# Kernel optimization log

Measured on AMD Instinct MI355X. Metric: run time of the kernel, lower is better.

Reference implementation:

```python
import jax, jax.numpy as jnp
import numpy as np

LEVELS = 2
_H0 = jnp.array([0.0322231, -0.01260397, -0.09921954, 0.2978578,
                 0.80373875, 0.49761867, -0.02963553, -0.07576571], dtype=jnp.float32)
_H1 = _H0[::-1] * jnp.array([-1.0, 1.0] * 4, dtype=jnp.float32)  # db4 QMF


def subband_conv2d(x, kernel_2d, stride):
    # depthwise grouped conv: same 2D kernel applied to every channel
    C = x.shape[-1]
    k = jnp.tile(kernel_2d[:, :, None, None], (1, 1, 1, C))  # HWIO with I=1, groups=C
    return jax.lax.conv_general_dilated(
        x, k, window_strides=(stride, stride), padding='SAME',
        dimension_numbers=('NHWC', 'HWIO', 'NHWC'), feature_group_count=C)


def _upsample2d(t):
    B, H, W, C = t.shape
    return jnp.zeros((B, 2 * H, 2 * W, C), t.dtype).at[:, ::2, ::2, :].set(t)


def _local_conv(t, w):
    # per-spatial-position linear map over channels: [B,H,W,I] x [I,O,W,H] -> [B,H,W,O]
    return jnp.einsum('bhwi,iowh->bhwo', t, w)


def setup_inputs() -> dict:
    key = jax.random.key(0)
    ks = jax.random.split(key, 9)
    B, H, W, C, O = 16, 128, 128, 64, 64
    inp = {
        'x': jax.random.normal(ks[0], (B, H, W, C), dtype=jnp.float32),
        'wLL': 0.02 * jax.random.normal(ks[1], (C, O, 32, 32), dtype=jnp.float32),
        'wLH_l0': 0.02 * jax.random.normal(ks[2], (C, O, 64, 64), dtype=jnp.float32),
        'wHL_l0': 0.02 * jax.random.normal(ks[3], (C, O, 64, 64), dtype=jnp.float32),
        'wHH_l0': 0.02 * jax.random.normal(ks[4], (C, O, 64, 64), dtype=jnp.float32),
        'wLH_l1': 0.02 * jax.random.normal(ks[5], (C, O, 32, 32), dtype=jnp.float32),
        'wHL_l1': 0.02 * jax.random.normal(ks[6], (C, O, 32, 32), dtype=jnp.float32),
        'wHH_l1': 0.02 * jax.random.normal(ks[7], (C, O, 32, 32), dtype=jnp.float32),
    }
    return inp


def reference(x, wLL, wLH_l0, wHL_l0, wHH_l0, wLH_l1, wHL_l1, wHH_l1):
    h0, h1 = _H0, _H1
    g0, g1 = h0[::-1], h1[::-1]
    # H=W=128 is divisible by 2**levels, so no symmetric padding is needed.
    res = x
    details = []
    for _ in range(LEVELS):
        cLL = subband_conv2d(res, jnp.outer(h0, h0), 2)
        cLH = subband_conv2d(res, jnp.outer(h0, h1), 2)
        cHL = subband_conv2d(res, jnp.outer(h1, h0), 2)
        cHH = subband_conv2d(res, jnp.outer(h1, h1), 2)
        details.append((cLH, cHL, cHH))
        res = cLL
    yA = _local_conv(res, wLL)  # [B,32,32,O]
    det_w = [(wLH_l0, wHL_l0, wHH_l0), (wLH_l1, wHL_l1, wHH_l1)]
    td = []
    for i in range(LEVELS):
        lh, hl, hh = details[i]
        wlh, whl, whh = det_w[i]
        td.append((_local_conv(lh, wlh), _local_conv(hl, whl), _local_conv(hh, whh)))
    r = yA
    for i in reversed(range(LEVELS)):
        yLH, yHL, yHH = td[i]
        r = (subband_conv2d(_upsample2d(r), jnp.outer(g0, g0), 1)
             + subband_conv2d(_upsample2d(yLH), jnp.outer(g0, g1), 1)
             + subband_conv2d(_upsample2d(yHL), jnp.outer(g1, g0), 1)
             + subband_conv2d(_upsample2d(yHH), jnp.outer(g1, g1), 1))
    return r
```

## Files before the change

### kernel.cpp

```cpp
#include <hip/hip_runtime.h>

__device__ __constant__ float H0[8] = { 0.0322231f, -0.01260397f, -0.09921954f,  0.2978578f,
                                        0.80373875f, 0.49761867f, -0.02963553f, -0.07576571f};
__device__ __constant__ float H1[8] = { 0.07576571f, -0.02963553f, -0.49761867f, 0.80373875f,
                                       -0.2978578f, -0.09921954f,  0.01260397f,  0.0322231f};
__device__ __constant__ float G0[8] = {-0.07576571f, -0.02963553f,  0.49761867f, 0.80373875f,
                                        0.2978578f,  -0.09921954f, -0.01260397f, 0.0322231f};
__device__ __constant__ float G1[8] = { 0.0322231f,   0.01260397f, -0.09921954f, -0.2978578f,
                                        0.80373875f, -0.49761867f, -0.02963553f, 0.07576571f};

template<int HIN>
__global__ __launch_bounds__(256) void fwd_dwt(const float* __restrict__ in,
                                               float* __restrict__ oLL, float* __restrict__ oLH,
                                               float* __restrict__ oHL, float* __restrict__ oHH)
{
    constexpr int OH = HIN / 2;
    constexpr int TQ = OH / 2;
    const int tid = threadIdx.x;
    const int c = tid & 63;
    const int s = blockIdx.x * 4 + (tid >> 6);
    const int j = s % TQ;
    const int i = (s / TQ) % TQ;
    const int b = s / (TQ * TQ);

    float acc[2][2][4];
#pragma unroll
    for (int a = 0; a < 2; ++a)
#pragma unroll
        for (int d = 0; d < 2; ++d)
#pragma unroll
            for (int k = 0; k < 4; ++k) acc[a][d][k] = 0.f;

    const int iw0 = 4 * j - 3;
#pragma unroll
    for (int r = 0; r < 10; ++r) {
        const int ih = 4 * i + r - 3;
        if ((unsigned)ih < (unsigned)HIN) {
            const float* row = in + ((b * HIN + ih) * HIN) * 64 + c;
            float xv[10];
#pragma unroll
            for (int v = 0; v < 10; ++v) {
                const int iw = iw0 + v;
                xv[v] = ((unsigned)iw < (unsigned)HIN) ? row[iw * 64] : 0.f;
            }
            float h00 = 0.f, h01 = 0.f, h10 = 0.f, h11 = 0.f;
#pragma unroll
            for (int v = 0; v < 8; ++v) {
                h00 += H0[v] * xv[v];
                h10 += H1[v] * xv[v];
                h01 += H0[v] * xv[v + 2];
                h11 += H1[v] * xv[v + 2];
            }
#pragma unroll
            for (int ii = 0; ii < 2; ++ii) {
                const int u = r - 2 * ii;
                if (0 <= u && u < 8) {
                    const float a0 = H0[u], a1 = H1[u];
                    acc[ii][0][0] += a0 * h00;
                    acc[ii][0][1] += a0 * h10;
                    acc[ii][0][2] += a1 * h00;
                    acc[ii][0][3] += a1 * h10;
                    acc[ii][1][0] += a0 * h01;
                    acc[ii][1][1] += a0 * h11;
                    acc[ii][1][2] += a1 * h01;
                    acc[ii][1][3] += a1 * h11;
                }
            }
        }
    }

#pragma unroll
    for (int ii = 0; ii < 2; ++ii)
#pragma unroll
        for (int jj = 0; jj < 2; ++jj) {
            const int oh = 2 * i + ii, ow = 2 * j + jj;
            const int oidx = ((b * OH + oh) * OH + ow) * 64 + c;
            oLL[oidx] = acc[ii][jj][0];
            oLH[oidx] = acc[ii][jj][1];
            oHL[oidx] = acc[ii][jj][2];
            oHH[oidx] = acc[ii][jj][3];
        }
}

template<int HD>
__global__ __launch_bounds__(256) void act_tr(const float* __restrict__ in,
                                              float* __restrict__ outp)
{
    __shared__ float Ld[64][HD + 1];
    const int w = blockIdx.x;
    const int b = blockIdx.y;
    const int t = threadIdx.x;

    {
        const int i = t & 63;
        const int hq = t >> 6;
#pragma unroll
        for (int s = 0; s < HD / 4; ++s) {
            const int h = hq * (HD / 4) + s;
            Ld[i][h] = in[((size_t)(b * HD + h) * HD + w) * 64 + i];
        }
    }
    __syncthreads();
    {
        const int h = t & (HD - 1);
        const int iq = t / HD;
        constexpr int NIQ = 256 / HD;
#pragma unroll
        for (int s = 0; s < 64 / NIQ; ++s) {
            const int i = s * NIQ + iq;
            outp[((size_t)(w * 64 + i) * 16 + b) * HD + h] = Ld[i][h];
        }
    }
}

template<int HD, int OT, int HG>
__global__ __launch_bounds__(256, 4) void local_conv_t(
    const float* __restrict__ a0, const float* __restrict__ a1,
    const float* __restrict__ a2, const float* __restrict__ a3,
    const float* __restrict__ w0, const float* __restrict__ w1,
    const float* __restrict__ w2, const float* __restrict__ w3,
    float* __restrict__ o0, float* __restrict__ o1,
    float* __restrict__ o2, float* __restrict__ o3)
{
    constexpr int WH   = HD * HD;
    constexpr int NO   = OT / 4;
    constexpr int WL   = OT / 8;
    constexpr int LOG2OT = (OT == 32) ? 5 : 4;
    constexpr int RSW  = OT + 4;
    constexpr int RSA  = 20;

    __shared__ __align__(16) float Wl[4][32][RSW];
    __shared__ __align__(16) float Al[4][32][RSA];

    const int z = blockIdx.z;
    const float* act = (z == 0) ? a0 : (z == 1) ? a1 : (z == 2) ? a2 : a3;
    const float* wgt = (z == 0) ? w0 : (z == 1) ? w1 : (z == 2) ? w2 : w3;
    float*       out = (z == 0) ? o0 : (z == 1) ? o1 : (z == 2) ? o2 : o3;

    const int bx    = blockIdx.x;
    const int hg    = bx % HG;
    const int og    = bx / HG;
    const int hbase = hg * 32;
    const int w     = blockIdx.y;
    const int t     = threadIdx.x;

    int whq[WL], wot[WL], wii[WL];
#pragma unroll
    for (int l = 0; l < WL; ++l) {
        const int idx = t + 256 * l;
        whq[l] = idx & 7;
        wot[l] = (idx >> 3) & (OT - 1);
        wii[l] = idx >> (3 + LOG2OT);
    }
    const int ahq = t & 7, ab = (t >> 3) & 15, aii0 = t >> 7;

    const int hc = t & 31;
    const int r  = t >> 5;
    const int oo = r & 3;
    const int bq = r >> 2;

    float4 acc4[8][NO / 4];
#pragma unroll
    for (int j = 0; j < 8; ++j)
#pragma unroll
        for (int q = 0; q < NO / 4; ++q) acc4[j][q] = make_float4(0.f, 0.f, 0.f, 0.f);

    float4 wv[WL], av[2];
#pragma unroll
    for (int l = 0; l < WL; ++l)
        wv[l] = *(const float4*)(wgt + (size_t)(wii[l] * 64 + og * OT + wot[l]) * WH
                                 + w * HD + hbase + whq[l] * 4);
#pragma unroll
    for (int l = 0; l < 2; ++l)
        av[l] = *(const float4*)(act + (size_t)((w * 64 + aii0 + 2 * l) * 16 + ab) * HD
                                 + hbase + ahq * 4);

    for (int chunk = 0; chunk < 16; ++chunk) {
        __syncthreads();
#pragma unroll
        for (int l = 0; l < WL; ++l) {
            Wl[wii[l]][whq[l] * 4 + 0][wot[l]] = wv[l].x;
            Wl[wii[l]][whq[l] * 4 + 1][wot[l]] = wv[l].y;
            Wl[wii[l]][whq[l] * 4 + 2][wot[l]] = wv[l].z;
            Wl[wii[l]][whq[l] * 4 + 3][wot[l]] = wv[l].w;
        }
#pragma unroll
        for (int l = 0; l < 2; ++l) {
            const int ii = aii0 + 2 * l;
            Al[ii][ahq * 4 + 0][ab] = av[l].x;
            Al[ii][ahq * 4 + 1][ab] = av[l].y;
            Al[ii][ahq * 4 + 2][ab] = av[l].z;
            Al[ii][ahq * 4 + 3][ab] = av[l].w;
        }
        __syncthreads();

        if (chunk < 15) {
            const int i0n = (chunk + 1) * 4;
#pragma unroll
            for (int l = 0; l < WL; ++l)
                wv[l] = *(const float4*)(wgt + (size_t)((i0n + wii[l]) * 64 + og * OT + wot[l]) * WH
                                         + w * HD + hbase + whq[l] * 4);
#pragma unroll
            for (int l = 0; l < 2; ++l)
                av[l] = *(const float4*)(act + (size_t)((w * 64 + i0n + aii0 + 2 * l) * 16 + ab) * HD
                                         + hbase + ahq * 4);
        }

#pragma unroll
        for (int ii = 0; ii < 4; ++ii) {
            float4 wf[NO / 4];
#pragma unroll
            for (int q = 0; q < NO / 4; ++q)
                wf[q] = *(const float4*)&Wl[ii][hc][oo * NO + q * 4];
            float4 af0 = *(const float4*)&Al[ii][hc][bq * 8];
            float4 af1 = *(const float4*)&Al[ii][hc][bq * 8 + 4];
            const float* afp0 = (const float*)&af0;
            const float* afp1 = (const float*)&af1;
#pragma unroll
            for (int j = 0; j < 4; ++j) {
                const float aa = afp0[j];
#pragma unroll
                for (int q = 0; q < NO / 4; ++q) {
                    acc4[j][q].x += aa * wf[q].x;
                    acc4[j][q].y += aa * wf[q].y;
                    acc4[j][q].z += aa * wf[q].z;
                    acc4[j][q].w += aa * wf[q].w;
                }
            }
#pragma unroll
            for (int j = 0; j < 4; ++j) {
                const float aa = afp1[j];
#pragma unroll
                for (int q = 0; q < NO / 4; ++q) {
                    acc4[j + 4][q].x += aa * wf[q].x;
                    acc4[j + 4][q].y += aa * wf[q].y;
                    acc4[j + 4][q].z += aa * wf[q].z;
                    acc4[j + 4][q].w += aa * wf[q].w;
                }
            }
        }
    }

#pragma unroll
    for (int j = 0; j < 8; ++j) {
        const int b = bq * 8 + j;
        float* op = out + ((size_t)(b * HD + hbase + hc) * HD + w) * 64 + og * OT + oo * NO;
#pragma unroll
        for (int q = 0; q < NO / 4; ++q)
            *(float4*)(op + q * 4) = acc4[j][q];
    }
}

template<int HOUT>
__global__ __launch_bounds__(256) void inv_dwt(const float* __restrict__ yLL,
                                               const float* __restrict__ yLH,
                                               const float* __restrict__ yHL,
                                               const float* __restrict__ yHH,
                                               float* __restrict__ out)
{
    constexpr int HS = HOUT / 2;
    const int tid = threadIdx.x;
    const int c = tid & 63;
    const int s = blockIdx.x * 4 + (tid >> 6);
    const int j = s % HS;
    const int i = (s / HS) % HS;
    const int b = s / (HS * HS);

    float Pe[4] = {0.f, 0.f, 0.f, 0.f}, Po[4] = {0.f, 0.f, 0.f, 0.f};
    float Qe[4] = {0.f, 0.f, 0.f, 0.f}, Qo[4] = {0.f, 0.f, 0.f, 0.f};

#pragma unroll
    for (int ku = 0; ku < 4; ++ku) {
        const int m = i - 1 + ku;
        if ((unsigned)m < (unsigned)HS) {
            const float a0e = G0[1 + 2 * ku], a0o = G0[2 * ku];
            const float a1e = G1[1 + 2 * ku], a1o = G1[2 * ku];
            const int rowoff = (b * HS + m) * HS;
#pragma unroll
            for (int kv = 0; kv < 4; ++kv) {
                const int n = j - 1 + kv;
                if ((unsigned)n < (unsigned)HS) {
                    const int idx = (rowoff + n) * 64 + c;
                    const float yll = yLL[idx], ylh = yLH[idx];
                    const float yhl = yHL[idx], yhh = yHH[idx];
                    Pe[kv] += a0e * yll + a1e * yhl;
                    Po[kv] += a0o * yll + a1o * yhl;
                    Qe[kv] += a0e * ylh + a1e * yhh;
                    Qo[kv] += a0o * ylh + a1o * yhh;
                }
            }
        }
    }

    float o00 = 0.f, o01 = 0.f, o10 = 0.f, o11 = 0.f;
#pragma unroll
    for (int kv = 0; kv < 4; ++kv) {
        const float b0e = G0[1 + 2 * kv], b0o = G0[2 * kv];
        const float b1e = G1[1 + 2 * kv], b1o = G1[2 * kv];
        o00 += b0e * Pe[kv] + b1e * Qe[kv];
        o01 += b0o * Pe[kv] + b1o * Qe[kv];
        o10 += b0e * Po[kv] + b1e * Qo[kv];
        o11 += b0o * Po[kv] + b1o * Qo[kv];
    }

    const int h0 = 2 * i, w0 = 2 * j;
    const int base = ((b * HOUT + h0) * HOUT + w0) * 64 + c;
    out[base] = o00;
    out[base + 64] = o01;
    out[base + HOUT * 64] = o10;
    out[base + HOUT * 64 + 64] = o11;
}

extern "C" void kernel_launch(void* const* d_in, const int* in_sizes, int n_in,
                              void* d_out, int out_size, void* d_ws, size_t ws_size,
                              hipStream_t stream)
{
    const float* x    = (const float*)d_in[0];
    const float* wLL  = (const float*)d_in[1];
    const float* wLH0 = (const float*)d_in[2];
    const float* wHL0 = (const float*)d_in[3];
    const float* wHH0 = (const float*)d_in[4];
    const float* wLH1 = (const float*)d_in[5];
    const float* wHL1 = (const float*)d_in[6];
    const float* wHH1 = (const float*)d_in[7];
    float* out = (float*)d_out;
    float* ws  = (float*)d_ws;

    const int S0 = 16 * 64 * 64 * 64;
    const int S1 = 16 * 32 * 32 * 64;

    float* c0 = out;
    float* A0 = out;
    float* A1 = out + 3 * S0;

    float* c1 = ws;
    float* t0 = ws + 4 * S1;
    float* t1 = ws + 4 * S1 + 3 * S0;
    float* yA = ws + 7 * S1 + 3 * S0;
    float* r1 = ws;

    fwd_dwt<128><<<16 * 32 * 32 / 4, 256, 0, stream>>>(x, c0, c0 + S0, c0 + 2 * S0, c0 + 3 * S0);

    fwd_dwt<64><<<16 * 16 * 16 / 4, 256, 0, stream>>>(c0,
        c1 + 0 * S1, c1 + 1 * S1, c1 + 2 * S1, c1 + 3 * S1);

    act_tr<64><<<dim3(64, 16), 256, 0, stream>>>(c0 + 1 * S0, A0 + 0 * S0);
    act_tr<64><<<dim3(64, 16), 256, 0, stream>>>(c0 + 2 * S0, A0 + 1 * S0);
    act_tr<64><<<dim3(64, 16), 256, 0, stream>>>(c0 + 3 * S0, A0 + 2 * S0);

    act_tr<32><<<dim3(32, 16), 256, 0, stream>>>(c1 + 0 * S1, A1 + 0 * S1);
    act_tr<32><<<dim3(32, 16), 256, 0, stream>>>(c1 + 1 * S1, A1 + 1 * S1);
    act_tr<32><<<dim3(32, 16), 256, 0, stream>>>(c1 + 2 * S1, A1 + 2 * S1);
    act_tr<32><<<dim3(32, 16), 256, 0, stream>>>(c1 + 3 * S1, A1 + 3 * S1);

    local_conv_t<64, 32, 2><<<dim3(4, 64, 3), 256, 0, stream>>>(
        A0 + 0 * S0, A0 + 1 * S0, A0 + 2 * S0, nullptr,
        wLH0, wHL0, wHH0, nullptr,
        t0 + 0 * S0, t0 + 1 * S0, t0 + 2 * S0, nullptr);

    local_conv_t<32, 16, 1><<<dim3(4, 32, 4), 256, 0, stream>>>(
        A1 + 1 * S1, A1 + 2 * S1, A1 + 3 * S1, A1 + 0 * S1,
        wLH1, wHL1, wHH1, wLL,
        t1 + 0 * S1, t1 + 1 * S1, t1 + 2 * S1, yA);

    inv_dwt<64><<<16 * 32 * 32 / 4, 256, 0, stream>>>(
        yA, t1 + 0 * S1, t1 + 1 * S1, t1 + 2 * S1, r1);

    inv_dwt<128><<<16 * 64 * 64 / 4, 256, 0, stream>>>(
        r1, t0 + 0 * S0, t0 + 1 * S0, t0 + 2 * S0, out);
}
```

Baseline: 333.0 us.

## Replace LDS-staged local conv with direct register loads and LDS-transposed stores

The per-position channel-mixing kernel no longer stages weight and activation tiles through shared memory with double-buffered prefetch. Each thread now loads its weights and activations straight from global memory with coalesced scalar loads along h and accumulates in registers. The result is transposed through a padded shared buffer so output stores stay coalesced. Level-0 output tiling drops from 32 to 16 channels per block, doubling the grid. This removes LDS traffic and per-chunk barriers, but loses register-level data reuse and the overlap of loads with compute.

```diff
diff --git a/kernel.cpp b/kernel.cpp
--- a/kernel.cpp
+++ b/kernel.cpp
@@ -114,7 +114,7 @@
 }
 
 template<int HD, int OT, int HG>
-__global__ __launch_bounds__(256, 4) void local_conv_t(
+__global__ __launch_bounds__(256) void local_conv_direct(
     const float* __restrict__ a0, const float* __restrict__ a1,
     const float* __restrict__ a2, const float* __restrict__ a3,
     const float* __restrict__ w0, const float* __restrict__ w1,
@@ -122,15 +122,15 @@
     float* __restrict__ o0, float* __restrict__ o1,
     float* __restrict__ o2, float* __restrict__ o3)
 {
-    constexpr int WH   = HD * HD;
-    constexpr int NO   = OT / 4;
-    constexpr int WL   = OT / 8;
-    constexpr int LOG2OT = (OT == 32) ? 5 : 4;
-    constexpr int RSW  = OT + 4;
-    constexpr int RSA  = 20;
-
-    __shared__ __align__(16) float Wl[4][32][RSW];
-    __shared__ __align__(16) float Al[4][32][RSA];
+    constexpr int WH  = HD * HD;
+    constexpr int NOO = OT / 8;
+    constexpr int NBQ = 8 / NOO;
+    constexpr int NB  = 16 / NBQ;
+    constexpr int NO4 = OT / 4;
+    constexpr int NEX = 256 / (NO4 * 32);
+    constexpr int NF  = NB / NEX;
+
+    __shared__ float E[NB][32][33];
 
     const int z = blockIdx.z;
     const float* act = (z == 0) ? a0 : (z == 1) ? a1 : (z == 2) ? a2 : a3;
@@ -144,110 +144,67 @@
     const int w     = blockIdx.y;
     const int t     = threadIdx.x;
 
-    int whq[WL], wot[WL], wii[WL];
-#pragma unroll
-    for (int l = 0; l < WL; ++l) {
-        const int idx = t + 256 * l;
-        whq[l] = idx & 7;
-        wot[l] = (idx >> 3) & (OT - 1);
-        wii[l] = idx >> (3 + LOG2OT);
-    }
-    const int ahq = t & 7, ab = (t >> 3) & 15, aii0 = t >> 7;
-
     const int hc = t & 31;
     const int r  = t >> 5;
-    const int oo = r & 3;
-    const int bq = r >> 2;
-
-    float4 acc4[8][NO / 4];
-#pragma unroll
-    for (int j = 0; j < 8; ++j)
-#pragma unroll
-        for (int q = 0; q < NO / 4; ++q) acc4[j][q] = make_float4(0.f, 0.f, 0.f, 0.f);
-
-    float4 wv[WL], av[2];
-#pragma unroll
-    for (int l = 0; l < WL; ++l)
-        wv[l] = *(const float4*)(wgt + (size_t)(wii[l] * 64 + og * OT + wot[l]) * WH
-                                 + w * HD + hbase + whq[l] * 4);
-#pragma unroll
-    for (int l = 0; l < 2; ++l)
-        av[l] = *(const float4*)(act + (size_t)((w * 64 + aii0 + 2 * l) * 16 + ab) * HD
-                                 + hbase + ahq * 4);
+    const int oo = r & (NOO - 1);
+    const int bq = r / NOO;
+
+    const float* wp = wgt + (size_t)(og * OT + oo * 8) * WH + w * HD + hbase + hc;
+    const float* ap = act + ((size_t)(w * 64) * 16 + bq * NB) * HD + hbase + hc;
+
+    float acc[NB][8];
+#pragma unroll
+    for (int j = 0; j < NB; ++j)
+#pragma unroll
+        for (int q = 0; q < 8; ++q) acc[j][q] = 0.f;
 
     for (int chunk = 0; chunk < 16; ++chunk) {
+        float wr[4][8];
+        float ar[4][NB];
+#pragma unroll
+        for (int i = 0; i < 4; ++i) {
+            const int ig = chunk * 4 + i;
+#pragma unroll
+            for (int q = 0; q < 8; ++q)
+                wr[i][q] = wp[(size_t)(ig * 64 + q) * WH];
+#pragma unroll
+            for (int j = 0; j < NB; ++j)
+                ar[i][j] = ap[(size_t)(ig * 16 + j) * HD];
+        }
+#pragma unroll
+        for (int i = 0; i < 4; ++i)
+#pragma unroll
+            for (int j = 0; j < NB; ++j) {
+                const float a = ar[i][j];
+#pragma unroll
+                for (int q = 0; q < 8; ++q)
+                    acc[j][q] += a * wr[i][q];
+            }
+    }
+
+    const int oF  = t & (NO4 - 1);
+    const int hcF = (t / NO4) & 31;
+    const int ex  = t / (NO4 * 32);
+
+    for (int p = 0; p < NBQ; ++p) {
+        if (p) __syncthreads();
+        if (bq == p) {
+#pragma unroll
+            for (int j = 0; j < NB; ++j)
+#pragma unroll
+                for (int q = 0; q < 8; ++q)
+                    E[j][hc][oo * 8 + q] = acc[j][q];
+        }
         __syncthreads();
 #pragma unroll
-        for (int l = 0; l < WL; ++l) {
-            Wl[wii[l]][whq[l] * 4 + 0][wot[l]] = wv[l].x;
-            Wl[wii[l]][whq[l] * 4 + 1][wot[l]] = wv[l].y;
-            Wl[wii[l]][whq[l] * 4 + 2][wot[l]] = wv[l].z;
-            Wl[wii[l]][whq[l] * 4 + 3][wot[l]] = wv[l].w;
-        }
-#pragma unroll
-        for (int l = 0; l < 2; ++l) {
-            const int ii = aii0 + 2 * l;
-            Al[ii][ahq * 4 + 0][ab] = av[l].x;
-            Al[ii][ahq * 4 + 1][ab] = av[l].y;
-            Al[ii][ahq * 4 + 2][ab] = av[l].z;
-            Al[ii][ahq * 4 + 3][ab] = av[l].w;
-        }
-        __syncthreads();
-
-        if (chunk < 15) {
-            const int i0n = (chunk + 1) * 4;
-#pragma unroll
-            for (int l = 0; l < WL; ++l)
-                wv[l] = *(const float4*)(wgt + (size_t)((i0n + wii[l]) * 64 + og * OT + wot[l]) * WH
-                                         + w * HD + hbase + whq[l] * 4);
-#pragma unroll
-            for (int l = 0; l < 2; ++l)
-                av[l] = *(const float4*)(act + (size_t)((w * 64 + i0n + aii0 + 2 * l) * 16 + ab) * HD
-                                         + hbase + ahq * 4);
-        }
-
-#pragma unroll
-        for (int ii = 0; ii < 4; ++ii) {
-            float4 wf[NO / 4];
-#pragma unroll
-            for (int q = 0; q < NO / 4; ++q)
-                wf[q] = *(const float4*)&Wl[ii][hc][oo * NO + q * 4];
-            float4 af0 = *(const float4*)&Al[ii][hc][bq * 8];
-            float4 af1 = *(const float4*)&Al[ii][hc][bq * 8 + 4];
-            const float* afp0 = (const float*)&af0;
-            const float* afp1 = (const float*)&af1;
-#pragma unroll
-            for (int j = 0; j < 4; ++j) {
-                const float aa = afp0[j];
-#pragma unroll
-                for (int q = 0; q < NO / 4; ++q) {
-                    acc4[j][q].x += aa * wf[q].x;
-                    acc4[j][q].y += aa * wf[q].y;
-                    acc4[j][q].z += aa * wf[q].z;
-                    acc4[j][q].w += aa * wf[q].w;
-                }
-            }
-#pragma unroll
-            for (int j = 0; j < 4; ++j) {
-                const float aa = afp1[j];
-#pragma unroll
-                for (int q = 0; q < NO / 4; ++q) {
-                    acc4[j + 4][q].x += aa * wf[q].x;
-                    acc4[j + 4][q].y += aa * wf[q].y;
-                    acc4[j + 4][q].z += aa * wf[q].z;
-                    acc4[j + 4][q].w += aa * wf[q].w;
-                }
-            }
-        }
-    }
-
-#pragma unroll
-    for (int j = 0; j < 8; ++j) {
-        const int b = bq * 8 + j;
-        float* op = out + ((size_t)(b * HD + hbase + hc) * HD + w) * 64 + og * OT + oo * NO;
-#pragma unroll
-        for (int q = 0; q < NO / 4; ++q)
-            *(float4*)(op + q * 4) = acc4[j][q];
+        for (int f = 0; f < NF; ++f) {
+            const int bi = ex + f * NEX;
+            float4 v = make_float4(E[bi][hcF][oF * 4 + 0], E[bi][hcF][oF * 4 + 1],
+                                   E[bi][hcF][oF * 4 + 2], E[bi][hcF][oF * 4 + 3]);
+            const int b = p * NB + bi;
+            *(float4*)(out + ((size_t)(b * HD + hbase + hcF) * HD + w) * 64
+                       + og * OT + oF * 4) = v;
+        }
     }
 }
 
@@ -353,12 +310,12 @@
     act_tr<32><<<dim3(32, 16), 256, 0, stream>>>(c1 + 2 * S1, A1 + 2 * S1);
     act_tr<32><<<dim3(32, 16), 256, 0, stream>>>(c1 + 3 * S1, A1 + 3 * S1);
 
-    local_conv_t<64, 32, 2><<<dim3(4, 64, 3), 256, 0, stream>>>(
+    local_conv_direct<64, 16, 2><<<dim3(8, 64, 3), 256, 0, stream>>>(
         A0 + 0 * S0, A0 + 1 * S0, A0 + 2 * S0, nullptr,
         wLH0, wHL0, wHH0, nullptr,
         t0 + 0 * S0, t0 + 1 * S0, t0 + 2 * S0, nullptr);
 
-    local_conv_t<32, 16, 1><<<dim3(4, 32, 4), 256, 0, stream>>>(
+    local_conv_direct<32, 16, 1><<<dim3(4, 32, 4), 256, 0, stream>>>(
         A1 + 1 * S1, A1 + 2 * S1, A1 + 3 * S1, A1 + 0 * S1,
         wLH1, wHL1, wHH1, wLL,
         t1 + 0 * S1, t1 + 1 * S1, t1 + 2 * S1, yA);
```

After: 337.2 us. Within noise of the previous version (+1.3%).
